# Optimization experiments

Hardware: AMD Instinct MI355X
Metric: run time of the kernel (lower is better)

## Reference

```python
import jax, jax.numpy as jnp
import numpy as np
from jax import lax

START_TAG_IDX = 1
NUM_TAGS = 64
END_TAG_IDX = NUM_TAGS - 1
NEG_INF = -10000.0


def _forward_alg(feats, mask, transitions):
    # feats: (B, S, N), mask: (B, S) float, transitions: (N, N)
    B, S, N = feats.shape
    init = jnp.full((B, N), NEG_INF, dtype=feats.dtype).at[:, START_TAG_IDX].set(0.0)

    def step(fv, xs):
        emit, m = xs  # (B, N), (B,)
        # logsumexp over previous tag: fv[b, prev] + T[prev, next]
        nv = jax.nn.logsumexp(fv[:, :, None] + transitions[None, :, :], axis=1) + emit
        m = m[:, None]
        fv = m * nv + (1.0 - m) * fv
        return fv, None

    fv, _ = lax.scan(step, init, (jnp.swapaxes(feats, 0, 1), mask.T))
    terminal = fv + transitions[:, END_TAG_IDX][None, :]
    return jax.nn.logsumexp(terminal, axis=1)  # (B,)


def _score_sentence(feats, mask, tags, transitions):
    B, S, N = feats.shape
    start = jnp.full((B, 1), START_TAG_IDX, dtype=tags.dtype)
    tags_ext = jnp.concatenate([start, tags], axis=1)  # (B, S+1)
    # emission score at gold tags, masked
    emit = jnp.take_along_axis(feats, tags[:, :, None], axis=2)[:, :, 0]  # (B, S)
    # transition score tags[i] -> tags[i+1], masked
    trans = transitions[tags_ext[:, :-1], tags_ext[:, 1:]]  # (B, S)
    score = jnp.sum((emit + trans) * mask, axis=1)
    # transition from last real tag to END
    seq_ends = mask.sum(axis=1).astype(jnp.int32) - 1  # (B,)
    last_tags = tags_ext[jnp.arange(B), seq_ends + 1]
    return score + transitions[last_tags, END_TAG_IDX]


def reference(feats, mask, tags, transitions):
    forward_score = _forward_alg(feats, mask, transitions)
    gold_score = _score_sentence(feats, mask, tags, transitions)
    return jnp.mean(forward_score - gold_score)  # average_batch=True


def setup_inputs() -> dict:
    key = jax.random.key(0)
    k1, k2, k3 = jax.random.split(key, 3)
    B, S, N = 512, 512, NUM_TAGS
    feats = jax.random.normal(k1, (B, S, N), dtype=jnp.float32)
    mask = jnp.ones((B, S), dtype=jnp.float32)
    tags = jax.random.randint(k2, (B, S), 0, N).astype(jnp.int64)
    transitions = jax.random.uniform(k3, (N, N), dtype=jnp.float32, minval=-0.1, maxval=0.1)
    return {"feats": feats, "mask": mask, "tags": tags, "transitions": transitions}
```

## Files before the change

### kernel.cpp

```cpp
#include <hip/hip_runtime.h>
#include <hip/hip_bf16.h>

#define NTAGS 64
#define START_TAG 1
#define END_TAG 63
#define LN2F 0.69314718055994530942f
#define NSEG 16

typedef float v4f __attribute__((ext_vector_type(4)));
typedef short s16x8 __attribute__((ext_vector_type(8)));

static __device__ __forceinline__ unsigned short f2bfu(float x) {
    union { __hip_bfloat16 h; unsigned short s; } u;
    u.h = __float2bfloat16(x);
    return u.s;
}
static __device__ __forceinline__ unsigned int packbf(float lo, float hi) {
    return (unsigned int)f2bfu(lo) | ((unsigned int)f2bfu(hi) << 16);
}
static __device__ __forceinline__ float xor16_get(float send) {
#if __has_builtin(__builtin_amdgcn_permlane16_swap)
    auto rr = __builtin_amdgcn_permlane16_swap(__float_as_uint(send), __float_as_uint(send),
                                               false, false);
    return (__uint_as_float((unsigned)rr[0]) + __uint_as_float((unsigned)rr[1])) - send;
#else
    return __shfl_xor(send, 16);
#endif
}
static __device__ __forceinline__ float xor32_get(float send) {
#if __has_builtin(__builtin_amdgcn_permlane32_swap)
    auto rr = __builtin_amdgcn_permlane32_swap(__float_as_uint(send), __float_as_uint(send),
                                               false, false);
    return (__uint_as_float((unsigned)rr[0]) + __uint_as_float((unsigned)rr[1])) - send;
#else
    return __shfl_xor(send, 32);
#endif
}
static __device__ __forceinline__ v4f max4(v4f a, v4f b) {
    return __builtin_elementwise_max(a, b);
}

template <bool FWD>
static __device__ __forceinline__ void run_seg_mfma(
    const float* __restrict__ feats, const float* __restrict__ mask,
    const float* __restrict__ trans, float* __restrict__ outv,
    int* __restrict__ oute, int S, int t_begin, int L, int b0, int init_mode,
    unsigned int* __restrict__ lds) {
    const int lane = threadIdx.x & 63;
    const int c = lane & 15, g = lane >> 4;
    const int swz = c & 7;

    s16x8 Af[4][2];
#pragma unroll
    for (int m = 0; m < 4; ++m)
#pragma unroll
        for (int kk = 0; kk < 2; ++kk)
#pragma unroll
            for (int e = 0; e < 8; ++e) {
                float tv = FWD ? trans[(32 * kk + 8 * g + e) * NTAGS + 16 * m + c]
                               : trans[(16 * m + c) * NTAGS + 32 * kk + 8 * g + e];
                Af[m][kk][e] = (short)f2bfu(__expf(tv));
            }

    v4f D[4];
    if (init_mode == 0) {
#pragma unroll
        for (int m = 0; m < 4; ++m) D[m] = (v4f){0.f, 0.f, 0.f, 0.f};
        if (g == 0) D[0].y = 1.0f;
    } else if (init_mode == 1) {
#pragma unroll
        for (int m = 0; m < 4; ++m) D[m] = (v4f){1.f, 1.f, 1.f, 1.f};
    } else {
#pragma unroll
        for (int m = 0; m < 4; ++m) {
            D[m].x = __expf(trans[(16 * m + 4 * g + 0) * NTAGS + END_TAG]);
            D[m].y = __expf(trans[(16 * m + 4 * g + 1) * NTAGS + END_TAG]);
            D[m].z = __expf(trans[(16 * m + 4 * g + 2) * NTAGS + END_TAG]);
            D[m].w = __expf(trans[(16 * m + 4 * g + 3) * NTAGS + END_TAG]);
        }
    }

    const float* fb = feats + (size_t)(b0 + c) * S * NTAGS;
    const float* mb = mask + (size_t)(b0 + c) * S;
    int esum = 0;

#define TT(sv) (FWD ? (t_begin + (sv)) : (t_begin + L - 1 - (sv)))
#define ELOAD(Ereg, Mreg, sv)                                                     \
    do {                                                                          \
        _Pragma("unroll") for (int n = 0; n < 4; ++n)                             \
            Ereg[n] = *(const v4f*)(fb + (size_t)TT(sv) * NTAGS + 16 * n + 4 * g);\
        Mreg = mb[TT(sv)];                                                        \
    } while (0)

#define STEPX(Ereg, Mv)                                                           \
    do {                                                                          \
        v4f Ex[4];                                                                \
        _Pragma("unroll") for (int n = 0; n < 4; ++n) {                           \
            Ex[n].x = __expf(Ereg[n].x); Ex[n].y = __expf(Ereg[n].y);             \
            Ex[n].z = __expf(Ereg[n].z); Ex[n].w = __expf(Ereg[n].w);             \
        }                                                                         \
        _Pragma("unroll") for (int n = 0; n < 4; ++n) {                           \
            v4f sv = FWD ? D[n] : D[n] * Ex[n];                                   \
            unsigned int u0 = packbf(sv.x, sv.y);                                 \
            unsigned int u1 = packbf(sv.z, sv.w);                                 \
            int G = 2 * n + (g >> 1);                                             \
            int di = c * 36 + ((G ^ swz) << 2) + 2 * (g & 1);                     \
            *reinterpret_cast<uint2*>(lds + di) = make_uint2(u0, u1);             \
        }                                                                         \
        s16x8 Bf0, Bf1;                                                           \
        { int di = c * 36 + ((g ^ swz) << 2);       Bf0 = *(const s16x8*)(lds + di); } \
        { int di = c * 36 + (((4 + g) ^ swz) << 2); Bf1 = *(const s16x8*)(lds + di); } \
        v4f Dm[4];                                                                \
        _Pragma("unroll") for (int m = 0; m < 4; ++m) {                           \
            v4f z = (v4f){0.f, 0.f, 0.f, 0.f};                                    \
            Dm[m] = __builtin_amdgcn_mfma_f32_16x16x32_bf16(Af[m][0], Bf0, z, 0, 0, 0); \
            Dm[m] = __builtin_amdgcn_mfma_f32_16x16x32_bf16(Af[m][1], Bf1, Dm[m], 0, 0, 0); \
        }                                                                         \
        if (FWD) {                                                                \
            _Pragma("unroll") for (int m = 0; m < 4; ++m) Dm[m] = Dm[m] * Ex[m];  \
        }                                                                         \
        bool act = (Mv != 0.0f);                                                  \
        _Pragma("unroll") for (int m = 0; m < 4; ++m) D[m] = act ? Dm[m] : D[m];  \
    } while (0)

    v4f EA[4], EB[4], EC[4], ED[4];
    float MA, MB, MC, MD;
    ELOAD(EA, MA, 0);
    ELOAD(EB, MB, 1);

    for (int s = 0; s < L; s += 4) {
        ELOAD(EC, MC, s + 2);
        ELOAD(ED, MD, s + 3);
        STEPX(EA, MA);
        STEPX(EB, MB);
        if (s + 4 < L) {
            ELOAD(EA, MA, s + 4);
            ELOAD(EB, MB, s + 5);
        }
        STEPX(EC, MC);
        STEPX(ED, MD);
        if (((s + 4) & 7) == 0) {
            v4f mm = max4(max4(D[0], D[1]), max4(D[2], D[3]));
            float mx = fmaxf(fmaxf(mm.x, mm.y), fmaxf(mm.z, mm.w));
            mx = fmaxf(mx, xor16_get(mx));
            mx = fmaxf(mx, xor32_get(mx));
            int ex;
            (void)frexpf(mx, &ex);
#pragma unroll
            for (int m = 0; m < 4; ++m) {
                D[m].x = ldexpf(D[m].x, -ex);
                D[m].y = ldexpf(D[m].y, -ex);
                D[m].z = ldexpf(D[m].z, -ex);
                D[m].w = ldexpf(D[m].w, -ex);
            }
            esum += ex;
        }
    }
#undef STEPX
#undef ELOAD
#undef TT

    float* oc = outv + (size_t)(b0 + c) * NTAGS;
#pragma unroll
    for (int m = 0; m < 4; ++m) *(v4f*)(oc + 16 * m + 4 * g) = D[m];
    if (g == 0) oute[b0 + c] = esum;
}

__global__ __launch_bounds__(64) void crf_chains(const float* __restrict__ feats,
                                                 const float* __restrict__ mask,
                                                 const int* __restrict__ tags,
                                                 const float* __restrict__ trans,
                                                 float* __restrict__ seg,
                                                 int* __restrict__ es,
                                                 float* __restrict__ gs,
                                                 int S, int L, int B, int nchain) {
    const int bid = (int)blockIdx.x;
    const int lane = threadIdx.x;

    if (bid >= nchain) {
        const int b = bid - nchain;
        const float* fb = feats + (size_t)b * S * NTAGS;
        const float* mb = mask + (size_t)b * S;
        const int* tb = tags + (size_t)b * S;
        float acc = 0.f, msum = 0.f;
        for (int t = lane; t < S; t += 64) {
            int cur = tb[t];
            int prev = (t == 0) ? START_TAG : tb[t - 1];
            float m = mb[t];
            acc += (fb[t * NTAGS + cur] + trans[prev * NTAGS + cur]) * m;
            msum += m;
        }
#pragma unroll
        for (int sh = 32; sh >= 1; sh >>= 1) {
            acc += __shfl_xor(acc, sh);
            msum += __shfl_xor(msum, sh);
        }
        if (lane == 0) {
            int seq_end = (int)(msum + 0.5f) - 1;
            int last = (seq_end >= 0) ? tb[seq_end] : START_TAG;
            gs[b] = acc + trans[last * NTAGS + END_TAG];
        }
        return;
    }

    __shared__ unsigned int lds[16 * 36];
    const int ngrp = B / 16;
    const int type = bid / ngrp;
    const int grp = bid - type * ngrp;
    const int b0 = grp * 16;

    float* outv = seg + (size_t)type * B * NTAGS;
    int* oute = es + type * B;

    if (type < 15) {
        run_seg_mfma<true>(feats, mask, trans, outv, oute, S, type * L, L, b0,
                           (type == 0) ? 0 : 1, lds);
    } else {
        const int sg = type - 14;
        run_seg_mfma<false>(feats, mask, trans, outv, oute, S, sg * L, L, b0,
                            (sg == 15) ? 2 : 1, lds);
    }
}

__global__ __launch_bounds__(512) void crf_finish(const float* __restrict__ seg,
                                                  const int* __restrict__ es,
                                                  const float* __restrict__ gs,
                                                  float* __restrict__ scores, int B) {
    const int tid = threadIdx.x;
    const int wave = tid >> 6, lane = tid & 63;
    const int b = blockIdx.x * 8 + wave;
    if (b >= B) return;

    float rv[15], lv[15];
#pragma unroll
    for (int gi = 0; gi < 15; ++gi)
        rv[gi] = seg[((size_t)gi * B + b) * NTAGS + lane];
#pragma unroll
    for (int gi = 0; gi < 15; ++gi)
        lv[gi] = seg[((size_t)(15 + gi) * B + b) * NTAGS + lane];

    float d[15], sl[14];
#pragma unroll
    for (int gi = 0; gi < 15; ++gi) d[gi] = lv[gi] * rv[gi];
#pragma unroll
    for (int gi = 0; gi < 14; ++gi) sl[gi] = lv[gi];
#pragma unroll
    for (int sh = 32; sh >= 1; sh >>= 1) {
#pragma unroll
        for (int gi = 0; gi < 15; ++gi) d[gi] += __shfl_xor(d[gi], sh);
#pragma unroll
        for (int gi = 0; gi < 14; ++gi) sl[gi] += __shfl_xor(sl[gi], sh);
    }
    if (lane == 0) {
        int esum = es[29 * B + b];
#pragma unroll
        for (int gi = 0; gi < 15; ++gi) esum += es[gi * B + b];
        float score = (float)esum * LN2F;
#pragma unroll
        for (int gi = 0; gi < 15; ++gi) score += __logf(d[gi]);
#pragma unroll
        for (int gi = 0; gi < 14; ++gi) score -= __logf(sl[gi]);
        scores[b] = score - gs[b];
    }
}

__global__ __launch_bounds__(1024) void crf_mean(const float* __restrict__ scores,
                                                 float* __restrict__ out, int B) {
    const int tid = threadIdx.x;
    float a = 0.f;
    for (int i = tid; i < B; i += 1024) a += scores[i];
#pragma unroll
    for (int sh = 32; sh >= 1; sh >>= 1) a += __shfl_xor(a, sh);
    __shared__ float buf[16];
    if ((tid & 63) == 0) buf[tid >> 6] = a;
    __syncthreads();
    if (tid == 0) {
        float s = 0.f;
#pragma unroll
        for (int i = 0; i < 16; ++i) s += buf[i];
        out[0] = s / (float)B;
    }
}

extern "C" void kernel_launch(void* const* d_in, const int* in_sizes, int n_in,
                              void* d_out, int out_size, void* d_ws, size_t ws_size,
                              hipStream_t stream) {
    const float* feats = (const float*)d_in[0];
    const float* mask  = (const float*)d_in[1];
    const int*   tags  = (const int*)d_in[2];
    const float* trans = (const float*)d_in[3];
    float* out = (float*)d_out;

    const int S = 512;
    const int B = in_sizes[1] / S;
    const int L = S / NSEG;
    const int nchain = 30 * (B / 16);

    float* seg = (float*)d_ws;
    int* es = (int*)(seg + (size_t)30 * B * NTAGS);
    float* gs = (float*)(es + 30 * B);
    float* scores = gs + B;

    crf_chains<<<nchain + B, 64, 0, stream>>>(feats, mask, tags, trans,
                                              seg, es, gs, S, L, B, nchain);
    crf_finish<<<(B + 7) / 8, 512, 0, stream>>>(seg, es, gs, scores, B);
    crf_mean<<<1, 1024, 0, stream>>>(scores, out, B);
}
```

Baseline: 40.53 us.

## Double segment count to 32 and replace LDS transpose with permlane swaps

Splits the sequence into 32 segments instead of 16, so 62 chain types run in parallel and each serial chain is half as long. The per-step LDS write/read transpose that builds the MFMA B operand is replaced with permlane32/permlane16 swap instructions held in registers. The finish kernel is restructured so each lane handles one segment junction with a vectorised dot product, followed by a single wave reduction. The cost is more blocks, more workspace traffic and more combine work.

```diff
diff --git a/kernel.cpp b/kernel.cpp
--- a/kernel.cpp
+++ b/kernel.cpp
@@ -5,7 +5,7 @@
 #define START_TAG 1
 #define END_TAG 63
 #define LN2F 0.69314718055994530942f
-#define NSEG 16
+#define NSEG 32
 
 typedef float v4f __attribute__((ext_vector_type(4)));
 typedef short s16x8 __attribute__((ext_vector_type(8)));
@@ -19,22 +19,14 @@
     return (unsigned int)f2bfu(lo) | ((unsigned int)f2bfu(hi) << 16);
 }
 static __device__ __forceinline__ float xor16_get(float send) {
-#if __has_builtin(__builtin_amdgcn_permlane16_swap)
     auto rr = __builtin_amdgcn_permlane16_swap(__float_as_uint(send), __float_as_uint(send),
                                                false, false);
     return (__uint_as_float((unsigned)rr[0]) + __uint_as_float((unsigned)rr[1])) - send;
-#else
-    return __shfl_xor(send, 16);
-#endif
 }
 static __device__ __forceinline__ float xor32_get(float send) {
-#if __has_builtin(__builtin_amdgcn_permlane32_swap)
     auto rr = __builtin_amdgcn_permlane32_swap(__float_as_uint(send), __float_as_uint(send),
                                                false, false);
     return (__uint_as_float((unsigned)rr[0]) + __uint_as_float((unsigned)rr[1])) - send;
-#else
-    return __shfl_xor(send, 32);
-#endif
 }
 static __device__ __forceinline__ v4f max4(v4f a, v4f b) {
     return __builtin_elementwise_max(a, b);
@@ -44,11 +36,9 @@
 static __device__ __forceinline__ void run_seg_mfma(
     const float* __restrict__ feats, const float* __restrict__ mask,
     const float* __restrict__ trans, float* __restrict__ outv,
-    int* __restrict__ oute, int S, int t_begin, int L, int b0, int init_mode,
-    unsigned int* __restrict__ lds) {
+    int* __restrict__ oute, int S, int t_begin, int L, int b0, int init_mode) {
     const int lane = threadIdx.x & 63;
     const int c = lane & 15, g = lane >> 4;
-    const int swz = c & 7;
 
     s16x8 Af[4][2];
 #pragma unroll
@@ -94,27 +84,35 @@
 
 #define STEPX(Ereg, Mv)                                                           \
     do {                                                                          \
-        v4f Ex[4];                                                                \
+        v4f Ex[4];                                                               \
         _Pragma("unroll") for (int n = 0; n < 4; ++n) {                           \
             Ex[n].x = __expf(Ereg[n].x); Ex[n].y = __expf(Ereg[n].y);             \
             Ex[n].z = __expf(Ereg[n].z); Ex[n].w = __expf(Ereg[n].w);             \
         }                                                                         \
+        unsigned int up[4][2];                                                    \
         _Pragma("unroll") for (int n = 0; n < 4; ++n) {                           \
             v4f sv = FWD ? D[n] : D[n] * Ex[n];                                   \
-            unsigned int u0 = packbf(sv.x, sv.y);                                 \
-            unsigned int u1 = packbf(sv.z, sv.w);                                 \
-            int G = 2 * n + (g >> 1);                                             \
-            int di = c * 36 + ((G ^ swz) << 2) + 2 * (g & 1);                     \
-            *reinterpret_cast<uint2*>(lds + di) = make_uint2(u0, u1);             \
-        }                                                                         \
-        s16x8 Bf0, Bf1;                                                           \
-        { int di = c * 36 + ((g ^ swz) << 2);       Bf0 = *(const s16x8*)(lds + di); } \
-        { int di = c * 36 + (((4 + g) ^ swz) << 2); Bf1 = *(const s16x8*)(lds + di); } \
+            up[n][0] = packbf(sv.x, sv.y);                                        \
+            up[n][1] = packbf(sv.z, sv.w);                                        \
+        }                                                                         \
+        union { unsigned int d[4]; s16x8 v; } bf0, bf1;                           \
+        {                                                                         \
+            auto rA = __builtin_amdgcn_permlane32_swap(up[0][0], up[1][0], false, false); \
+            auto rB = __builtin_amdgcn_permlane32_swap(up[0][1], up[1][1], false, false); \
+            auto rC = __builtin_amdgcn_permlane32_swap(up[2][0], up[3][0], false, false); \
+            auto rD = __builtin_amdgcn_permlane32_swap(up[2][1], up[3][1], false, false); \
+            auto sA = __builtin_amdgcn_permlane16_swap((unsigned)rA[0], (unsigned)rA[1], false, false); \
+            auto sB = __builtin_amdgcn_permlane16_swap((unsigned)rB[0], (unsigned)rB[1], false, false); \
+            auto sC = __builtin_amdgcn_permlane16_swap((unsigned)rC[0], (unsigned)rC[1], false, false); \
+            auto sD = __builtin_amdgcn_permlane16_swap((unsigned)rD[0], (unsigned)rD[1], false, false); \
+            bf0.d[0] = sA[0]; bf0.d[1] = sB[0]; bf0.d[2] = sA[1]; bf0.d[3] = sB[1]; \
+            bf1.d[0] = sC[0]; bf1.d[1] = sD[0]; bf1.d[2] = sC[1]; bf1.d[3] = sD[1]; \
+        }                                                                         \
         v4f Dm[4];                                                                \
         _Pragma("unroll") for (int m = 0; m < 4; ++m) {                           \
             v4f z = (v4f){0.f, 0.f, 0.f, 0.f};                                    \
-            Dm[m] = __builtin_amdgcn_mfma_f32_16x16x32_bf16(Af[m][0], Bf0, z, 0, 0, 0); \
-            Dm[m] = __builtin_amdgcn_mfma_f32_16x16x32_bf16(Af[m][1], Bf1, Dm[m], 0, 0, 0); \
+            Dm[m] = __builtin_amdgcn_mfma_f32_16x16x32_bf16(Af[m][0], bf0.v, z, 0, 0, 0); \
+            Dm[m] = __builtin_amdgcn_mfma_f32_16x16x32_bf16(Af[m][1], bf1.v, Dm[m], 0, 0, 0); \
         }                                                                         \
         if (FWD) {                                                                \
             _Pragma("unroll") for (int m = 0; m < 4; ++m) Dm[m] = Dm[m] * Ex[m];  \
@@ -203,7 +201,6 @@
         return;
     }
 
-    __shared__ unsigned int lds[16 * 36];
     const int ngrp = B / 16;
     const int type = bid / ngrp;
     const int grp = bid - type * ngrp;
@@ -212,13 +209,13 @@
     float* outv = seg + (size_t)type * B * NTAGS;
     int* oute = es + type * B;
 
-    if (type < 15) {
+    if (type < 31) {
         run_seg_mfma<true>(feats, mask, trans, outv, oute, S, type * L, L, b0,
-                           (type == 0) ? 0 : 1, lds);
+                           (type == 0) ? 0 : 1);
     } else {
-        const int sg = type - 14;
+        const int sg = type - 30;
         run_seg_mfma<false>(feats, mask, trans, outv, oute, S, sg * L, L, b0,
-                            (sg == 15) ? 2 : 1, lds);
+                            (sg == 31) ? 2 : 1);
     }
 }
 
@@ -231,37 +228,30 @@
     const int b = blockIdx.x * 8 + wave;
     if (b >= B) return;
 
-    float rv[15], lv[15];
-#pragma unroll
-    for (int gi = 0; gi < 15; ++gi)
-        rv[gi] = seg[((size_t)gi * B + b) * NTAGS + lane];
-#pragma unroll
-    for (int gi = 0; gi < 15; ++gi)
-        lv[gi] = seg[((size_t)(15 + gi) * B + b) * NTAGS + lane];
-
-    float d[15], sl[14];
-#pragma unroll
-    for (int gi = 0; gi < 15; ++gi) d[gi] = lv[gi] * rv[gi];
-#pragma unroll
-    for (int gi = 0; gi < 14; ++gi) sl[gi] = lv[gi];
-#pragma unroll
-    for (int sh = 32; sh >= 1; sh >>= 1) {
-#pragma unroll
-        for (int gi = 0; gi < 15; ++gi) d[gi] += __shfl_xor(d[gi], sh);
-#pragma unroll
-        for (int gi = 0; gi < 14; ++gi) sl[gi] += __shfl_xor(sl[gi], sh);
-    }
-    if (lane == 0) {
-        int esum = es[29 * B + b];
-#pragma unroll
-        for (int gi = 0; gi < 15; ++gi) esum += es[gi * B + b];
-        float score = (float)esum * LN2F;
-#pragma unroll
-        for (int gi = 0; gi < 15; ++gi) score += __logf(d[gi]);
-#pragma unroll
-        for (int gi = 0; gi < 14; ++gi) score -= __logf(sl[gi]);
-        scores[b] = score - gs[b];
-    }
+    float contrib = 0.f;
+    if (lane < 31) {
+        const int g = lane + 1;
+        const float* rv = seg + ((size_t)(g - 1) * B + b) * NTAGS;
+        const float* lv = seg + ((size_t)(30 + g) * B + b) * NTAGS;
+        v4f dacc = (v4f){0.f, 0.f, 0.f, 0.f};
+        v4f sacc = dacc;
+#pragma unroll
+        for (int i = 0; i < 16; ++i) {
+            v4f rr = *(const v4f*)(rv + 4 * i);
+            v4f ll = *(const v4f*)(lv + 4 * i);
+            dacc = __builtin_elementwise_fma(ll, rr, dacc);
+            sacc = sacc + ll;
+        }
+        float dot = (dacc.x + dacc.y) + (dacc.z + dacc.w);
+        float sl = (sacc.x + sacc.y) + (sacc.z + sacc.w);
+        contrib = __logf(dot) + (float)es[(size_t)(g - 1) * B + b] * LN2F;
+        if (g <= 30) contrib -= __logf(sl);
+    } else if (lane == 31) {
+        contrib = (float)es[(size_t)61 * B + b] * LN2F;
+    }
+#pragma unroll
+    for (int sh = 32; sh >= 1; sh >>= 1) contrib += __shfl_xor(contrib, sh);
+    if (lane == 0) scores[b] = contrib - gs[b];
 }
 
 __global__ __launch_bounds__(1024) void crf_mean(const float* __restrict__ scores,
@@ -294,11 +284,11 @@
     const int S = 512;
     const int B = in_sizes[1] / S;
     const int L = S / NSEG;
-    const int nchain = 30 * (B / 16);
+    const int nchain = 62 * (B / 16);
 
     float* seg = (float*)d_ws;
-    int* es = (int*)(seg + (size_t)30 * B * NTAGS);
-    float* gs = (float*)(es + 30 * B);
+    int* es = (int*)(seg + (size_t)62 * B * NTAGS);
+    float* gs = (float*)(es + 62 * B);
     float* scores = gs + B;
 
     crf_chains<<<nchain + B, 64, 0, stream>>>(feats, mask, tags, trans,
```

New measurement: 42.63 us. +5.2%, slower.
